# Performance work log

Measured on AMD Instinct MI355X. Metric: run time of the kernel, lower is better.

The kernel has to match this reference:

```python
import jax, jax.numpy as jnp
import numpy as np

N_CLASSES = 8  # hardcoded by the (-1, 8, 8) reshape in the original layer

def setup_inputs() -> dict:
    key = jax.random.key(0)
    k1, k2, k3, k4 = jax.random.split(key, 4)
    B, F, C, R = 16384, 128, N_CLASSES, 64
    x = jax.random.normal(k1, (B, F), dtype=jnp.float32)
    p = jax.random.uniform(k2, (B, C), dtype=jnp.float32)  # class-prob-like input
    W = jax.random.normal(k3, (F, C * C, R), dtype=jnp.float32) * 0.02
    b = jax.random.normal(k4, (C, C, R), dtype=jnp.float32) * 0.1
    return {"x": x, "p": p, "W": W, "b": b}

def reference(x, p, W, b):
    # x: (B, 128) features; p: (B, C) class probs; W: (128, C*C, R); b: (C, C, R)
    B = x.shape[0]
    C = b.shape[0]
    R = b.shape[-1]
    # per-annotator GEMM fused across all annotators: (B, C*C, R)
    logits = jnp.einsum('bf,fkr->bkr', x, W).reshape(B, C, C, R) + b[None]
    # row-softmax: softmax over the "predicted class" axis for each true class c
    M = jax.nn.softmax(logits, axis=2)  # (B, C, C, R)
    # batched dot: p (B,C) contracted against rows of each annotator matrix
    out = jnp.einsum('bc,bcdr->bdr', p, M)  # (B, C, R)
    # NOTE: original applies K.dropout(0.5) (training-mode); omitted for a
    # deterministic inference reference (identity at eval).
    return out
```

## Files before the change

### kernel.cpp

```cpp
#include <hip/hip_runtime.h>
#include <hip/hip_bf16.h>


#define B_ROWS   16384
#define F_DIM    128
#define NCOL     4096
#define OUT_STRIDE 512
#define LOG2E    1.44269504088896340736f

typedef __bf16 bf16x8 __attribute__((ext_vector_type(8)));
typedef float  f32x4  __attribute__((ext_vector_type(4)));

#define AS1(p) ((const __attribute__((address_space(1))) unsigned int*)(p))
#define AS3(p) ((__attribute__((address_space(3))) unsigned int*)(p))

__global__ void wconv_kernel(const float* __restrict__ W, __bf16* __restrict__ wf) {
    int f    = blockIdx.x * 256 + threadIdx.x;
    int lane = f & 63;
    int tkk  = f >> 6;
    int t    = tkk >> 2;
    int kk   = tkk & 3;
    int kbase = kk * 32 + (lane >> 4) * 8;
    int n     = t * 16 + (lane & 15);
    bf16x8 frag;
#pragma unroll
    for (int j = 0; j < 8; ++j)
        frag[j] = (__bf16)W[(kbase + j) * NCOL + n];
    *(bf16x8*)(wf + (size_t)f * 8) = frag;
}

__global__ __launch_bounds__(512, 4)
void fused_kernel(const float* __restrict__ x, const float* __restrict__ p,
                  const float* __restrict__ bias, const __bf16* __restrict__ wf,
                  float* __restrict__ out) {
    __shared__ __align__(16) char lds[65536];

    const int lane = threadIdx.x & 63;
    const int ww   = threadIdx.x >> 6;
    const int quad = lane >> 4;
    const int l15  = lane & 15;
    const int w    = blockIdx.x >> 7;
    const int g    = blockIdx.x & 127;
    const int b0   = g * 128 + ww * 16;

    {
        const __bf16* src = wf + (size_t)(((0 * 8 + ww) * 4 + w) * 4) * 512 + lane * 8;
#pragma unroll
        for (int kk = 0; kk < 4; ++kk)
            __builtin_amdgcn_global_load_lds(
                AS1(src + kk * 512),
                AS3(lds + (ww * 4 + kk) * 1024), 16, 0, 0);
    }

    bf16x8 afr[4];
    {
        const float* xr = x + (size_t)(b0 + l15) * F_DIM + quad * 8;
#pragma unroll
        for (int kk = 0; kk < 4; ++kk) {
            float4 lo = *(const float4*)(xr + kk * 32);
            float4 hi = *(const float4*)(xr + kk * 32 + 4);
            bf16x8 f;
            f[0] = (__bf16)lo.x; f[1] = (__bf16)lo.y;
            f[2] = (__bf16)lo.z; f[3] = (__bf16)lo.w;
            f[4] = (__bf16)hi.x; f[5] = (__bf16)hi.y;
            f[6] = (__bf16)hi.z; f[7] = (__bf16)hi.w;
            afr[kk] = f;
        }
    }

    float O[8][4] = {};

#pragma unroll 1
    for (int c = 0; c < 8; ++c) {
        __syncthreads();

        if (c < 7) {
            const __bf16* src =
                wf + (size_t)((((c + 1) * 8 + ww) * 4 + w) * 4) * 512 + lane * 8;
            char* dst = lds + ((c + 1) & 1) * 32768;
#pragma unroll
            for (int kk = 0; kk < 4; ++kk)
                __builtin_amdgcn_global_load_lds(
                    AS1(src + kk * 512),
                    AS3(dst + (ww * 4 + kk) * 1024), 16, 0, 0);
        }

        float pvv[4];
#pragma unroll
        for (int jj = 0; jj < 4; ++jj)
            pvv[jj] = p[(size_t)(b0 + quad * 4 + jj) * 8 + c];

        float bvl[8];
#pragma unroll
        for (int d = 0; d < 8; ++d)
            bvl[d] = bias[(c * 8 + d) * 64 + w * 16 + l15];

        f32x4 acc[8];
#pragma unroll
        for (int d = 0; d < 8; ++d) {
            f32x4 binit = {bvl[d], bvl[d], bvl[d], bvl[d]};
            acc[d] = binit;
        }

        const char* buf = lds + (c & 1) * 32768;
#pragma unroll
        for (int kk = 0; kk < 4; ++kk) {
            bf16x8 bfr[8];
#pragma unroll
            for (int d = 0; d < 8; ++d)
                bfr[d] = *(const bf16x8*)(buf + (d * 4 + kk) * 1024 + lane * 16);
#pragma unroll
            for (int d = 0; d < 8; ++d)
                acc[d] = __builtin_amdgcn_mfma_f32_16x16x32_bf16(
                             afr[kk], bfr[d], acc[d], 0, 0, 0);
        }

#pragma unroll
        for (int jj = 0; jj < 4; ++jj) {
            float e[8];
#pragma unroll
            for (int d = 0; d < 8; ++d)
                e[d] = __builtin_amdgcn_exp2f(acc[d][jj] * LOG2E);
            float s01 = e[0] + e[1], s23 = e[2] + e[3];
            float s45 = e[4] + e[5], s67 = e[6] + e[7];
            float s = (s01 + s23) + (s45 + s67);
            float scale = pvv[jj] * __builtin_amdgcn_rcpf(s);
#pragma unroll
            for (int d = 0; d < 8; ++d)
                O[d][jj] = __builtin_fmaf(e[d], scale, O[d][jj]);
        }
    }

#pragma unroll
    for (int jj = 0; jj < 4; ++jj) {
        float* orow = out + (size_t)(b0 + quad * 4 + jj) * OUT_STRIDE + w * 16 + l15;
#pragma unroll
        for (int d = 0; d < 8; ++d)
            orow[d * 64] = O[d][jj];
    }
}

extern "C" void kernel_launch(void* const* d_in, const int* in_sizes, int n_in,
                              void* d_out, int out_size, void* d_ws, size_t ws_size,
                              hipStream_t stream) {
    const float* x    = (const float*)d_in[0];
    const float* p    = (const float*)d_in[1];
    const float* W    = (const float*)d_in[2];
    const float* bias = (const float*)d_in[3];
    float* out = (float*)d_out;
    __bf16* wf = (__bf16*)d_ws;

    wconv_kernel<<<dim3(256), dim3(256), 0, stream>>>(W, wf);
    fused_kernel<<<dim3(512), dim3(512), 0, stream>>>(x, p, bias, wf, out);
}
```

Baseline: 99.43 us.

## Give each wave two 16-row M tiles to reuse B fragments across MFMAs

Halves the block to 4 waves of 256 threads, with each wave now covering 32 batch rows as two 16-row MFMA tiles. Each B fragment read from LDS feeds two MFMAs, halving LDS read traffic per MFMA. The weight slab staging is redistributed so each wave loads two d-slices. The costs are fewer waves per block and double the accumulator and output registers, which may reduce occupancy and latency hiding.

After: 101.4 us. 2.0% more time.

```diff
diff --git a/kernel.cpp b/kernel.cpp
--- a/kernel.cpp
+++ b/kernel.cpp
@@ -29,7 +29,7 @@
     *(bf16x8*)(wf + (size_t)f * 8) = frag;
 }
 
-__global__ __launch_bounds__(512, 4)
+__global__ __launch_bounds__(256, 2)
 void fused_kernel(const float* __restrict__ x, const float* __restrict__ p,
                   const float* __restrict__ bias, const __bf16* __restrict__ wf,
                   float* __restrict__ out) {
@@ -41,20 +41,24 @@
     const int l15  = lane & 15;
     const int w    = blockIdx.x >> 7;
     const int g    = blockIdx.x & 127;
-    const int b0   = g * 128 + ww * 16;
+    const int b0   = g * 128 + ww * 32;
 
     {
-        const __bf16* src = wf + (size_t)(((0 * 8 + ww) * 4 + w) * 4) * 512 + lane * 8;
 #pragma unroll
-        for (int kk = 0; kk < 4; ++kk)
+        for (int j = 0; j < 8; ++j) {
+            int d  = ww * 2 + (j >> 2);
+            int kk = j & 3;
+            int gf = d * 16 + w * 4 + kk;
             __builtin_amdgcn_global_load_lds(
-                AS1(src + kk * 512),
-                AS3(lds + (ww * 4 + kk) * 1024), 16, 0, 0);
+                AS1(wf + (size_t)gf * 512 + lane * 8),
+                AS3(lds + (d * 4 + kk) * 1024), 16, 0, 0);
+        }
     }
 
-    bf16x8 afr[4];
-    {
-        const float* xr = x + (size_t)(b0 + l15) * F_DIM + quad * 8;
+    bf16x8 afr[2][4];
+#pragma unroll
+    for (int m = 0; m < 2; ++m) {
+        const float* xr = x + (size_t)(b0 + m * 16 + l15) * F_DIM + quad * 8;
 #pragma unroll
         for (int kk = 0; kk < 4; ++kk) {
             float4 lo = *(const float4*)(xr + kk * 32);
@@ -64,80 +68,91 @@
             f[2] = (__bf16)lo.z; f[3] = (__bf16)lo.w;
             f[4] = (__bf16)hi.x; f[5] = (__bf16)hi.y;
             f[6] = (__bf16)hi.z; f[7] = (__bf16)hi.w;
-            afr[kk] = f;
+            afr[m][kk] = f;
         }
     }
 
-    float O[8][4] = {};
+    float O[2][8][4] = {};
 
 #pragma unroll 1
     for (int c = 0; c < 8; ++c) {
         __syncthreads();
 
         if (c < 7) {
-            const __bf16* src =
-                wf + (size_t)((((c + 1) * 8 + ww) * 4 + w) * 4) * 512 + lane * 8;
             char* dst = lds + ((c + 1) & 1) * 32768;
 #pragma unroll
-            for (int kk = 0; kk < 4; ++kk)
+            for (int j = 0; j < 8; ++j) {
+                int d  = ww * 2 + (j >> 2);
+                int kk = j & 3;
+                int gf = (c + 1) * 128 + d * 16 + w * 4 + kk;
                 __builtin_amdgcn_global_load_lds(
-                    AS1(src + kk * 512),
-                    AS3(dst + (ww * 4 + kk) * 1024), 16, 0, 0);
+                    AS1(wf + (size_t)gf * 512 + lane * 8),
+                    AS3(dst + (d * 4 + kk) * 1024), 16, 0, 0);
+            }
         }
 
-        float pvv[4];
+        float pvv[2][4];
 #pragma unroll
-        for (int jj = 0; jj < 4; ++jj)
-            pvv[jj] = p[(size_t)(b0 + quad * 4 + jj) * 8 + c];
+        for (int m = 0; m < 2; ++m)
+#pragma unroll
+            for (int jj = 0; jj < 4; ++jj)
+                pvv[m][jj] = p[(size_t)(b0 + m * 16 + quad * 4 + jj) * 8 + c];
 
         float bvl[8];
 #pragma unroll
         for (int d = 0; d < 8; ++d)
             bvl[d] = bias[(c * 8 + d) * 64 + w * 16 + l15];
 
-        f32x4 acc[8];
+        f32x4 acc[2][8];
 #pragma unroll
         for (int d = 0; d < 8; ++d) {
             f32x4 binit = {bvl[d], bvl[d], bvl[d], bvl[d]};
-            acc[d] = binit;
+            acc[0][d] = binit;
+            acc[1][d] = binit;
         }
 
         const char* buf = lds + (c & 1) * 32768;
 #pragma unroll
         for (int kk = 0; kk < 4; ++kk) {
-            bf16x8 bfr[8];
 #pragma unroll
-            for (int d = 0; d < 8; ++d)
-                bfr[d] = *(const bf16x8*)(buf + (d * 4 + kk) * 1024 + lane * 16);
-#pragma unroll
-            for (int d = 0; d < 8; ++d)
-                acc[d] = __builtin_amdgcn_mfma_f32_16x16x32_bf16(
-                             afr[kk], bfr[d], acc[d], 0, 0, 0);
+            for (int d = 0; d < 8; ++d) {
+                bf16x8 bfr = *(const bf16x8*)(buf + (d * 4 + kk) * 1024 + lane * 16);
+                acc[0][d] = __builtin_amdgcn_mfma_f32_16x16x32_bf16(
+                                afr[0][kk], bfr, acc[0][d], 0, 0, 0);
+                acc[1][d] = __builtin_amdgcn_mfma_f32_16x16x32_bf16(
+                                afr[1][kk], bfr, acc[1][d], 0, 0, 0);
+            }
         }
 
 #pragma unroll
-        for (int jj = 0; jj < 4; ++jj) {
-            float e[8];
+        for (int m = 0; m < 2; ++m) {
 #pragma unroll
-            for (int d = 0; d < 8; ++d)
-                e[d] = __builtin_amdgcn_exp2f(acc[d][jj] * LOG2E);
-            float s01 = e[0] + e[1], s23 = e[2] + e[3];
-            float s45 = e[4] + e[5], s67 = e[6] + e[7];
-            float s = (s01 + s23) + (s45 + s67);
-            float scale = pvv[jj] * __builtin_amdgcn_rcpf(s);
+            for (int jj = 0; jj < 4; ++jj) {
+                float e[8];
 #pragma unroll
-            for (int d = 0; d < 8; ++d)
-                O[d][jj] = __builtin_fmaf(e[d], scale, O[d][jj]);
+                for (int d = 0; d < 8; ++d)
+                    e[d] = __builtin_amdgcn_exp2f(acc[m][d][jj] * LOG2E);
+                float s01 = e[0] + e[1], s23 = e[2] + e[3];
+                float s45 = e[4] + e[5], s67 = e[6] + e[7];
+                float s = (s01 + s23) + (s45 + s67);
+                float scale = pvv[m][jj] * __builtin_amdgcn_rcpf(s);
+#pragma unroll
+                for (int d = 0; d < 8; ++d)
+                    O[m][d][jj] = __builtin_fmaf(e[d], scale, O[m][d][jj]);
+            }
         }
     }
 
 #pragma unroll
-    for (int jj = 0; jj < 4; ++jj) {
-        float* orow = out + (size_t)(b0 + quad * 4 + jj) * OUT_STRIDE + w * 16 + l15;
+    for (int m = 0; m < 2; ++m)
 #pragma unroll
-        for (int d = 0; d < 8; ++d)
-            orow[d * 64] = O[d][jj];
-    }
+        for (int jj = 0; jj < 4; ++jj) {
+            float* orow = out + (size_t)(b0 + m * 16 + quad * 4 + jj) * OUT_STRIDE
+                          + w * 16 + l15;
+#pragma unroll
+            for (int d = 0; d < 8; ++d)
+                orow[d * 64] = O[m][d][jj];
+        }
 }
 
 extern "C" void kernel_launch(void* const* d_in, const int* in_sizes, int n_in,
@@ -151,5 +166,5 @@
     __bf16* wf = (__bf16*)d_ws;
 
     wconv_kernel<<<dim3(256), dim3(256), 0, stream>>>(W, wf);
-    fused_kernel<<<dim3(512), dim3(512), 0, stream>>>(x, p, bias, wf, out);
+    fused_kernel<<<dim3(512), dim3(256), 0, stream>>>(x, p, bias, wf, out);
 }
```

## Halve block size, split each class step into two LDS half-stages, prescale by log2e

Applied to the files above, without the earlier changes.

The fused kernel now runs 256-thread blocks over 64 rows each, with twice as many blocks and half the LDS (32 KB). Each class iteration is split into two half-stages of four output columns. While one half's MFMAs run, the other half's weights stream into LDS, and the MFMA sections are wrapped in s_setprio. Weights and bias are prescaled by log2(e) in the conversion kernel, which removes a multiply before each exp2. The intent is higher occupancy and overlap of loads with compute, at the cost of an extra barrier per class and rounding of the prescaled weights to bf16.

Result: no change. 101.0 us (+1.6%).

```diff
diff --git a/kernel.cpp b/kernel.cpp
--- a/kernel.cpp
+++ b/kernel.cpp
@@ -14,7 +14,10 @@
 #define AS1(p) ((const __attribute__((address_space(1))) unsigned int*)(p))
 #define AS3(p) ((__attribute__((address_space(3))) unsigned int*)(p))
 
-__global__ void wconv_kernel(const float* __restrict__ W, __bf16* __restrict__ wf) {
+__global__ void wconv_kernel(const float* __restrict__ W,
+                             const float* __restrict__ bias,
+                             __bf16* __restrict__ wf,
+                             float* __restrict__ bias_s) {
     int f    = blockIdx.x * 256 + threadIdx.x;
     int lane = f & 63;
     int tkk  = f >> 6;
@@ -25,26 +28,28 @@
     bf16x8 frag;
 #pragma unroll
     for (int j = 0; j < 8; ++j)
-        frag[j] = (__bf16)W[(kbase + j) * NCOL + n];
+        frag[j] = (__bf16)(W[(kbase + j) * NCOL + n] * LOG2E);
     *(bf16x8*)(wf + (size_t)f * 8) = frag;
+    if (f < NCOL)
+        bias_s[f] = bias[f] * LOG2E;
 }
 
-__global__ __launch_bounds__(512, 4)
+__global__ __launch_bounds__(256, 4)
 void fused_kernel(const float* __restrict__ x, const float* __restrict__ p,
-                  const float* __restrict__ bias, const __bf16* __restrict__ wf,
+                  const float* __restrict__ bias_s, const __bf16* __restrict__ wf,
                   float* __restrict__ out) {
-    __shared__ __align__(16) char lds[65536];
+    __shared__ __align__(16) char lds[32768];
 
     const int lane = threadIdx.x & 63;
     const int ww   = threadIdx.x >> 6;
     const int quad = lane >> 4;
     const int l15  = lane & 15;
-    const int w    = blockIdx.x >> 7;
-    const int g    = blockIdx.x & 127;
-    const int b0   = g * 128 + ww * 16;
+    const int w    = blockIdx.x >> 8;
+    const int g    = blockIdx.x & 255;
+    const int b0   = g * 64 + ww * 16;
 
     {
-        const __bf16* src = wf + (size_t)(((0 * 8 + ww) * 4 + w) * 4) * 512 + lane * 8;
+        const __bf16* src = wf + (size_t)(ww * 16 + w * 4) * 512 + lane * 8;
 #pragma unroll
         for (int kk = 0; kk < 4; ++kk)
             __builtin_amdgcn_global_load_lds(
@@ -69,65 +74,98 @@
     }
 
     float O[8][4] = {};
+    f32x4 acc[8];
+    float pvv[4];
 
 #pragma unroll 1
     for (int c = 0; c < 8; ++c) {
-        __syncthreads();
+        {
+            __syncthreads();
 
-        if (c < 7) {
-            const __bf16* src =
-                wf + (size_t)((((c + 1) * 8 + ww) * 4 + w) * 4) * 512 + lane * 8;
-            char* dst = lds + ((c + 1) & 1) * 32768;
+            {
+                const __bf16* src =
+                    wf + (size_t)(c * 128 + (4 + ww) * 16 + w * 4) * 512 + lane * 8;
+#pragma unroll
+                for (int kk = 0; kk < 4; ++kk)
+                    __builtin_amdgcn_global_load_lds(
+                        AS1(src + kk * 512),
+                        AS3(lds + 16384 + (ww * 4 + kk) * 1024), 16, 0, 0);
+            }
+
+#pragma unroll
+            for (int jj = 0; jj < 4; ++jj)
+                pvv[jj] = p[(size_t)(b0 + quad * 4 + jj) * 8 + c];
+
+            float bvl[4];
+#pragma unroll
+            for (int dd = 0; dd < 4; ++dd)
+                bvl[dd] = bias_s[(c * 8 + dd) * 64 + w * 16 + l15];
+#pragma unroll
+            for (int dd = 0; dd < 4; ++dd) {
+                f32x4 binit = {bvl[dd], bvl[dd], bvl[dd], bvl[dd]};
+                acc[dd] = binit;
+            }
+
+            __builtin_amdgcn_s_setprio(1);
 #pragma unroll
             for (int kk = 0; kk < 4; ++kk)
-                __builtin_amdgcn_global_load_lds(
-                    AS1(src + kk * 512),
-                    AS3(dst + (ww * 4 + kk) * 1024), 16, 0, 0);
+#pragma unroll
+                for (int dd = 0; dd < 4; ++dd) {
+                    bf16x8 bfr = *(const bf16x8*)(lds + (dd * 4 + kk) * 1024 + lane * 16);
+                    acc[dd] = __builtin_amdgcn_mfma_f32_16x16x32_bf16(
+                                  afr[kk], bfr, acc[dd], 0, 0, 0);
+                }
+            __builtin_amdgcn_s_setprio(0);
         }
 
-        float pvv[4];
+        {
+            __syncthreads();
+
+            if (c < 7) {
+                const __bf16* src =
+                    wf + (size_t)((c + 1) * 128 + ww * 16 + w * 4) * 512 + lane * 8;
 #pragma unroll
-        for (int jj = 0; jj < 4; ++jj)
-            pvv[jj] = p[(size_t)(b0 + quad * 4 + jj) * 8 + c];
+                for (int kk = 0; kk < 4; ++kk)
+                    __builtin_amdgcn_global_load_lds(
+                        AS1(src + kk * 512),
+                        AS3(lds + (ww * 4 + kk) * 1024), 16, 0, 0);
+            }
 
-        float bvl[8];
+            float bvl[4];
 #pragma unroll
-        for (int d = 0; d < 8; ++d)
-            bvl[d] = bias[(c * 8 + d) * 64 + w * 16 + l15];
+            for (int dd = 0; dd < 4; ++dd)
+                bvl[dd] = bias_s[(c * 8 + 4 + dd) * 64 + w * 16 + l15];
+#pragma unroll
+            for (int dd = 0; dd < 4; ++dd) {
+                f32x4 binit = {bvl[dd], bvl[dd], bvl[dd], bvl[dd]};
+                acc[4 + dd] = binit;
+            }
 
-        f32x4 acc[8];
+            __builtin_amdgcn_s_setprio(1);
 #pragma unroll
-        for (int d = 0; d < 8; ++d) {
-            f32x4 binit = {bvl[d], bvl[d], bvl[d], bvl[d]};
-            acc[d] = binit;
-        }
-
-        const char* buf = lds + (c & 1) * 32768;
+            for (int kk = 0; kk < 4; ++kk)
 #pragma unroll
-        for (int kk = 0; kk < 4; ++kk) {
-            bf16x8 bfr[8];
-#pragma unroll
-            for (int d = 0; d < 8; ++d)
-                bfr[d] = *(const bf16x8*)(buf + (d * 4 + kk) * 1024 + lane * 16);
-#pragma unroll
-            for (int d = 0; d < 8; ++d)
-                acc[d] = __builtin_amdgcn_mfma_f32_16x16x32_bf16(
-                             afr[kk], bfr[d], acc[d], 0, 0, 0);
-        }
+                for (int dd = 0; dd < 4; ++dd) {
+                    bf16x8 bfr = *(const bf16x8*)(lds + 16384 + (dd * 4 + kk) * 1024 + lane * 16);
+                    acc[4 + dd] = __builtin_amdgcn_mfma_f32_16x16x32_bf16(
+                                      afr[kk], bfr, acc[4 + dd], 0, 0, 0);
+                }
+            __builtin_amdgcn_s_setprio(0);
 
 #pragma unroll
-        for (int jj = 0; jj < 4; ++jj) {
-            float e[8];
+            for (int jj = 0; jj < 4; ++jj) {
+                float e[8];
 #pragma unroll
-            for (int d = 0; d < 8; ++d)
-                e[d] = __builtin_amdgcn_exp2f(acc[d][jj] * LOG2E);
-            float s01 = e[0] + e[1], s23 = e[2] + e[3];
-            float s45 = e[4] + e[5], s67 = e[6] + e[7];
-            float s = (s01 + s23) + (s45 + s67);
-            float scale = pvv[jj] * __builtin_amdgcn_rcpf(s);
+                for (int d = 0; d < 8; ++d)
+                    e[d] = __builtin_amdgcn_exp2f(acc[d][jj]);
+                float s01 = e[0] + e[1], s23 = e[2] + e[3];
+                float s45 = e[4] + e[5], s67 = e[6] + e[7];
+                float s = (s01 + s23) + (s45 + s67);
+                float scale = pvv[jj] * __builtin_amdgcn_rcpf(s);
 #pragma unroll
-            for (int d = 0; d < 8; ++d)
-                O[d][jj] = __builtin_fmaf(e[d], scale, O[d][jj]);
+                for (int d = 0; d < 8; ++d)
+                    O[d][jj] = __builtin_fmaf(e[d], scale, O[d][jj]);
+            }
         }
     }
 
@@ -148,8 +186,9 @@
     const float* W    = (const float*)d_in[2];
     const float* bias = (const float*)d_in[3];
     float* out = (float*)d_out;
-    __bf16* wf = (__bf16*)d_ws;
+    __bf16* wf     = (__bf16*)d_ws;
+    float*  bias_s = (float*)((char*)d_ws + (1 << 20));
 
-    wconv_kernel<<<dim3(256), dim3(256), 0, stream>>>(W, wf);
-    fused_kernel<<<dim3(512), dim3(512), 0, stream>>>(x, p, bias, wf, out);
+    wconv_kernel<<<dim3(256), dim3(256), 0, stream>>>(W, bias, wf, bias_s);
+    fused_kernel<<<dim3(1024), dim3(256), 0, stream>>>(x, p, bias_s, wf, out);
 }
```
